# Kernel tuning notes

Hardware: AMD Instinct MI355X
Metric: run time of the kernel (lower is better)

Reference implementation:

```python
import jax, jax.numpy as jnp
import numpy as np

EMBED_DIM = 1024
NUM_HEADS = 16
HEAD_DIM = EMBED_DIM // NUM_HEADS
ROPE_BASE = 10000.0


def rotate_half(x):
    # interleaved variant: pairs (x0,x1) -> (-x1, x0)
    x1 = x[..., ::2]
    x2 = x[..., 1::2]
    return jnp.stack((-x2, x1), axis=-1).reshape(x.shape)


def rope_tables(T, dim, dtype):
    inv_freq = 1.0 / (ROPE_BASE ** (jnp.arange(0, dim, 2, dtype=jnp.float32) / dim))
    t = jnp.arange(T, dtype=jnp.float32)
    freqs = t[:, None] * inv_freq[None, :]          # [T, dim/2]
    emb = jnp.concatenate((freqs, freqs), axis=-1)  # [T, dim]
    return jnp.cos(emb).astype(dtype), jnp.sin(emb).astype(dtype)


def setup_inputs() -> dict:
    key = jax.random.key(0)
    kx, kq, ko = jax.random.split(key, 3)
    B, T, D = 2, 2048, EMBED_DIM
    x = jax.random.normal(kx, (B, T, D), dtype=jnp.float32)
    s = 1.0 / np.sqrt(D)
    Wqkv = jax.random.normal(kq, (D, 3 * D), dtype=jnp.float32) * s
    Wout = jax.random.normal(ko, (D, D), dtype=jnp.float32) * s
    return {"x": x, "Wqkv": Wqkv, "Wout": Wout}


def reference(x, Wqkv, Wout):
    B, T, D = x.shape
    H, hd = NUM_HEADS, HEAD_DIM
    qkv = x @ Wqkv                                   # [B,T,3D]
    q, k, v = jnp.split(qkv, 3, axis=-1)
    q = q.reshape(B, T, H, hd).transpose(0, 2, 1, 3)  # [B,H,T,hd]
    k = k.reshape(B, T, H, hd).transpose(0, 2, 1, 3)
    v = v.reshape(B, T, H, hd).transpose(0, 2, 1, 3)
    cos, sin = rope_tables(T, hd, x.dtype)           # [T,hd]
    cos = cos[None, None, :, :]
    sin = sin[None, None, :, :]
    q = q * cos + rotate_half(q) * sin
    k = k * cos + rotate_half(k) * sin
    scale = 1.0 / np.sqrt(hd).astype(np.float32)
    attn = jnp.einsum('bhtd,bhsd->bhts', q, k) * scale  # [B,H,T,T]
    attn = jax.nn.softmax(attn, axis=-1)
    out = jnp.einsum('bhts,bhsd->bhtd', attn, v)     # [B,H,T,hd]
    out = out.transpose(0, 2, 1, 3).reshape(B, T, D)
    return out @ Wout
```

## Files before the change

kernel.cpp:

```cpp
#include <hip/hip_runtime.h>
#include <hip/hip_bf16.h>
#include <stdint.h>


typedef unsigned short u16;
typedef short bf16x8 __attribute__((ext_vector_type(8)));
typedef float f32x4  __attribute__((ext_vector_type(4)));

#if defined(__has_builtin) && __has_builtin(__builtin_amdgcn_exp2f)
#define EXP2F(x) __builtin_amdgcn_exp2f(x)
#else
#define EXP2F(x) exp2f(x)
#endif

__device__ __forceinline__ u16 f2b(float f) {
  uint32_t u = __float_as_uint(f);
  u += 0x7fffu + ((u >> 16) & 1u);
  return (u16)(u >> 16);
}
__device__ __forceinline__ uint32_t pk2(float a, float b) {
  return (uint32_t)f2b(a) | ((uint32_t)f2b(b) << 16);
}

__device__ __forceinline__ void gl2lds16(const void* g, void* l) {
  __builtin_amdgcn_global_load_lds(
      (const __attribute__((address_space(1))) unsigned int*)g,
      (__attribute__((address_space(3))) unsigned int*)l, 16, 0, 0);
}

__global__ void sniff_kernel(const u16* x, int* flag) {
  __shared__ int cnt;
  if (threadIdx.x == 0) cnt = 0;
  __syncthreads();
  int c = 0;
  for (int i = threadIdx.x; i < 4096; i += 256) {
    float a = fabsf(__uint_as_float(((uint32_t)x[2*i]) << 16));
    if (a > 1e-3f && a < 100.f) c++;
  }
  atomicAdd(&cnt, c);
  __syncthreads();
  if (threadIdx.x == 0) *flag = (cnt > 2048) ? 1 : 0;
}

__global__ __launch_bounds__(256) void convert_x_kernel(
    const void* __restrict__ xv, const int* __restrict__ flag, u16* __restrict__ Xb)
{
  const int isb = *flag;
  const size_t i = ((size_t)blockIdx.x * 256 + threadIdx.x) * 8;
  if (isb) {
    *(uint4*)&Xb[i] = *(const uint4*)((const u16*)xv + i);
  } else {
    const float* s = (const float*)xv + i;
    float4 a = *(const float4*)s, b = *(const float4*)(s + 4);
    uint4 p;
    p.x = pk2(a.x, a.y); p.y = pk2(a.z, a.w);
    p.z = pk2(b.x, b.y); p.w = pk2(b.z, b.w);
    *(uint4*)&Xb[i] = p;
  }
}

__global__ __launch_bounds__(256) void transpose_w_kernel(
    const void* __restrict__ src, u16* __restrict__ dst,
    int K, int N, const int* __restrict__ flag)
{
  __shared__ u16 Lt[64 * 72];
  const int isb = *flag;
  const int tid = threadIdx.x;
  const int n0 = blockIdx.x * 64, k0 = blockIdx.y * 64;
  const int r = tid >> 2, cseg = (tid & 3) << 4;
  u16 t[16];
  if (isb) {
    const u16* s = (const u16*)src + (size_t)(k0 + r) * N + n0 + cseg;
    *(uint4*)&t[0] = *(const uint4*)s;
    *(uint4*)&t[8] = *(const uint4*)(s + 8);
  } else {
    const float* s = (const float*)src + (size_t)(k0 + r) * N + n0 + cseg;
    #pragma unroll
    for (int j = 0; j < 4; j++) {
      float4 v = *(const float4*)(s + j * 4);
      t[j*4+0] = f2b(v.x); t[j*4+1] = f2b(v.y); t[j*4+2] = f2b(v.z); t[j*4+3] = f2b(v.w);
    }
  }
  #pragma unroll
  for (int j = 0; j < 16; j++) Lt[(cseg + j) * 72 + r] = t[j];
  __syncthreads();
  const int n = tid >> 2, kseg = (tid & 3) << 4;
  uint4 u0 = *(const uint4*)&Lt[n * 72 + kseg];
  uint4 u1 = *(const uint4*)&Lt[n * 72 + kseg + 8];
  u16* d = dst + (size_t)(n0 + n) * K + k0 + kseg;
  *(uint4*)d = u0;
  *(uint4*)(d + 8) = u1;
}

__global__ __launch_bounds__(256) void rope_table_kernel(float2* __restrict__ CS) {
  const int idx = blockIdx.x * 256 + threadIdx.x;
  const int t = idx >> 5, f = idx & 31;
  float invf = __expf(-(float)f * 0.2878231366242557f);
  float th = (float)t * invf;
  float sn, cs;
  sincosf(th, &sn, &cs);
  CS[idx] = make_float2(cs, sn);
}

__global__ __launch_bounds__(256) void qkv_kernel(
    const u16* __restrict__ Xb, const u16* __restrict__ Wt,
    const float2* __restrict__ CS,
    u16* __restrict__ Q, u16* __restrict__ K, u16* __restrict__ Vt)
{
  __shared__ u16 As[128 * 64];
  __shared__ u16 Bs[128 * 64];
  const int tid = threadIdx.x;
  const int n0 = blockIdx.x * 128;
  const int m0 = blockIdx.y * 128;
  const int w = tid >> 6, l = tid & 63, lr = l & 15, lq = l >> 4;
  const int mrow0 = (w & 1) * 64;
  const int ncol0 = (w >> 1) * 64;

  const int srow = tid >> 3;
  const int gseg = (tid & 7) ^ (srow & 7);

  f32x4 acc[4][4] = {};

  for (int k0 = 0; k0 < 1024; k0 += 64) {
    __syncthreads();
    #pragma unroll
    for (int rd = 0; rd < 4; rd++) {
      const int row = srow + rd * 32;
      gl2lds16(Xb + (size_t)(m0 + row) * 1024 + k0 + gseg * 8, &As[tid * 8 + rd * 2048]);
      gl2lds16(Wt + (size_t)(n0 + row) * 1024 + k0 + gseg * 8, &Bs[tid * 8 + rd * 2048]);
    }
    __syncthreads();
    #pragma unroll
    for (int kc = 0; kc < 2; kc++) {
      bf16x8 af[4], bf[4];
      #pragma unroll
      for (int i = 0; i < 4; i++) {
        const int seg = ((kc << 2) | lq) ^ (lr & 7);
        af[i] = *(const bf16x8*)&As[(mrow0 + i * 16 + lr) * 64 + seg * 8];
        bf[i] = *(const bf16x8*)&Bs[(ncol0 + i * 16 + lr) * 64 + seg * 8];
      }
      #pragma unroll
      for (int mb = 0; mb < 4; mb++)
        #pragma unroll
        for (int nb = 0; nb < 4; nb++)
          acc[mb][nb] = __builtin_amdgcn_mfma_f32_16x16x32_bf16(af[mb], bf[nb], acc[mb][nb], 0, 0, 0);
    }
  }

  const int col0 = n0 + ncol0;
  const int sec = col0 >> 10;
  const int h = (col0 >> 6) & 15;
  if (sec == 2) {
    #pragma unroll
    for (int mb = 0; mb < 4; mb++) {
      const int row0 = m0 + mrow0 + mb * 16 + lq * 4;
      const int b = row0 >> 11, t0 = row0 & 2047;
      #pragma unroll
      for (int nb = 0; nb < 4; nb++) {
        const int d = nb * 16 + lr;
        uint2 uv;
        uv.x = pk2(acc[mb][nb][0], acc[mb][nb][1]);
        uv.y = pk2(acc[mb][nb][2], acc[mb][nb][3]);
        *(uint2*)&Vt[(((size_t)b * 16 + h) * 64 + d) * 2048 + t0] = uv;
      }
    }
  } else {
    u16* dst = (sec == 0) ? Q : K;
    const float qscale = 0.125f * 1.44269504f;
    #pragma unroll
    for (int mb = 0; mb < 4; mb++) {
      const int row0 = m0 + mrow0 + mb * 16 + lq * 4;
      const int b = row0 >> 11, t0 = row0 & 2047;
      #pragma unroll
      for (int nb = 0; nb < 4; nb++) {
        const int d = nb * 16 + lr;
        const int f = d & 31;
        #pragma unroll
        for (int r = 0; r < 4; r++) {
          const int t = t0 + r;
          float2 cs = CS[t * 32 + f];
          float val = acc[mb][nb][r];
          float prt = __shfl_xor(val, 1, 64);
          float res = fmaf(val, cs.x, ((d & 1) ? prt : -prt) * cs.y);
          if (sec == 0) res *= qscale;
          dst[(((size_t)b * 16 + h) * 2048 + t) * 64 + d] = f2b(res);
        }
      }
    }
  }
}

__global__ __launch_bounds__(256) void attn_kernel(
    const u16* __restrict__ Q, const u16* __restrict__ K,
    const u16* __restrict__ Vt, u16* __restrict__ ATT)
{
  __shared__ u16 Ks[64 * 64];
  __shared__ u16 Vs[64 * 64];
  __shared__ u16 Ps[4 * 32 * 72];
  const int tid = threadIdx.x;
  const int w = tid >> 6, l = tid & 63, lr = l & 15, lq = l >> 4;
  const int bh = blockIdx.x >> 4;
  const int qt = blockIdx.x & 15;
  const size_t base = (size_t)bh * (2048 * 64);
  const int qrow0 = qt * 128 + w * 32;
  u16* Psw = Ps + w * (32 * 72);

  bf16x8 qf[2][2];
  #pragma unroll
  for (int mb = 0; mb < 2; mb++)
    #pragma unroll
    for (int kc = 0; kc < 2; kc++)
      qf[mb][kc] = *(const bf16x8*)(Q + base + (size_t)(qrow0 + mb * 16 + lr) * 64 + kc * 32 + lq * 8);

  f32x4 oa[2][4] = {};
  f32x4 lsum[2] = {};

  const int srow = tid >> 3;
  const int gseg = (tid & 7) ^ (srow & 7);

  #pragma unroll 1
  for (int s0 = 0; s0 < 2048; s0 += 64) {
    __syncthreads();
    #pragma unroll
    for (int rd = 0; rd < 2; rd++) {
      const int row = srow + rd * 32;
      const int gs = (tid & 7) ^ (row & 7);
      gl2lds16(K + base + (size_t)(s0 + row) * 64 + gs * 8, &Ks[tid * 8 + rd * 2048]);
      gl2lds16(Vt + base + (size_t)row * 2048 + s0 + gs * 8, &Vs[tid * 8 + rd * 2048]);
    }
    __syncthreads();

    bf16x8 kf[4][2], vf[4][2];
    #pragma unroll
    for (int nb = 0; nb < 4; nb++)
      #pragma unroll
      for (int kc = 0; kc < 2; kc++) {
        const int seg = ((kc << 2) | lq) ^ (lr & 7);
        kf[nb][kc] = *(const bf16x8*)&Ks[(nb * 16 + lr) * 64 + seg * 8];
        vf[nb][kc] = *(const bf16x8*)&Vs[(nb * 16 + lr) * 64 + seg * 8];
      }

    const int ev = (lr & 1) == 0;
    #pragma unroll
    for (int mb = 0; mb < 2; mb++) {
      #pragma unroll
      for (int nb = 0; nb < 4; nb++) {
        f32x4 s = {};
        s = __builtin_amdgcn_mfma_f32_16x16x32_bf16(qf[mb][0], kf[nb][0], s, 0, 0, 0);
        s = __builtin_amdgcn_mfma_f32_16x16x32_bf16(qf[mb][1], kf[nb][1], s, 0, 0, 0);
        float e0 = EXP2F(s[0]), e1 = EXP2F(s[1]), e2 = EXP2F(s[2]), e3 = EXP2F(s[3]);
        lsum[mb][0] += e0; lsum[mb][1] += e1;
        lsum[mb][2] += e2; lsum[mb][3] += e3;
        uint32_t p01 = (uint32_t)f2b(e0) | ((uint32_t)f2b(e1) << 16);
        uint32_t p23 = (uint32_t)f2b(e2) | ((uint32_t)f2b(e3) << 16);
        uint32_t pp01 = (uint32_t)__shfl_xor((int)p01, 1, 64);
        uint32_t pp23 = (uint32_t)__shfl_xor((int)p23, 1, 64);
        uint32_t wA = ev ? ((p01 & 0xffffu) | (pp01 << 16))
                         : ((pp23 & 0xffffu) | (p23 << 16));
        uint32_t wB = ev ? ((p01 >> 16) | (pp01 & 0xffff0000u))
                         : ((pp23 >> 16) | (p23 & 0xffff0000u));
        const int row0 = mb * 16 + lq * 4 + (ev ? 0 : 2);
        const int c = nb * 16 + (lr & ~1);
        *(uint32_t*)&Psw[row0 * 72 + c] = wA;
        *(uint32_t*)&Psw[(row0 + 1) * 72 + c] = wB;
      }
    }

    #pragma unroll
    for (int mb = 0; mb < 2; mb++) {
      bf16x8 pf0 = *(const bf16x8*)&Psw[(mb * 16 + lr) * 72 + lq * 8];
      bf16x8 pf1 = *(const bf16x8*)&Psw[(mb * 16 + lr) * 72 + 32 + lq * 8];
      #pragma unroll
      for (int nb = 0; nb < 4; nb++) {
        oa[mb][nb] = __builtin_amdgcn_mfma_f32_16x16x32_bf16(pf0, vf[nb][0], oa[mb][nb], 0, 0, 0);
        oa[mb][nb] = __builtin_amdgcn_mfma_f32_16x16x32_bf16(pf1, vf[nb][1], oa[mb][nb], 0, 0, 0);
      }
    }
  }

  const int b = bh >> 4, h = bh & 15;
  #pragma unroll
  for (int mb = 0; mb < 2; mb++) {
    #pragma unroll
    for (int r = 0; r < 4; r++) {
      float v = lsum[mb][r];
      v += __shfl_xor(v, 1, 64);
      v += __shfl_xor(v, 2, 64);
      v += __shfl_xor(v, 4, 64);
      v += __shfl_xor(v, 8, 64);
      lsum[mb][r] = 1.f / v;
    }
    #pragma unroll
    for (int nb = 0; nb < 4; nb++) {
      const int d = nb * 16 + lr;
      #pragma unroll
      for (int r = 0; r < 4; r++) {
        const int t = qrow0 + mb * 16 + lq * 4 + r;
        ATT[((size_t)(b * 2048 + t)) * 1024 + h * 64 + d] = f2b(oa[mb][nb][r] * lsum[mb][r]);
      }
    }
  }
}

__global__ __launch_bounds__(256) void outproj_kernel(
    const u16* __restrict__ A, const u16* __restrict__ Wt,
    const int* __restrict__ flag, void* __restrict__ outv)
{
  __shared__ u16 As[128 * 64];
  __shared__ u16 Bs[128 * 64];
  const int isb = *flag;
  const int tid = threadIdx.x;
  const int n0 = blockIdx.x * 128;
  const int m0 = blockIdx.y * 128;
  const int w = tid >> 6, l = tid & 63, lr = l & 15, lq = l >> 4;
  const int mrow0 = (w & 1) * 64;
  const int ncol0 = (w >> 1) * 64;
  const int srow = tid >> 3;
  const int gseg = (tid & 7) ^ (srow & 7);

  f32x4 acc[4][4] = {};

  for (int k0 = 0; k0 < 1024; k0 += 64) {
    __syncthreads();
    #pragma unroll
    for (int rd = 0; rd < 4; rd++) {
      const int row = srow + rd * 32;
      gl2lds16(A + (size_t)(m0 + row) * 1024 + k0 + gseg * 8, &As[tid * 8 + rd * 2048]);
      gl2lds16(Wt + (size_t)(n0 + row) * 1024 + k0 + gseg * 8, &Bs[tid * 8 + rd * 2048]);
    }
    __syncthreads();
    #pragma unroll
    for (int kc = 0; kc < 2; kc++) {
      bf16x8 af[4], bf[4];
      #pragma unroll
      for (int i = 0; i < 4; i++) {
        const int seg = ((kc << 2) | lq) ^ (lr & 7);
        af[i] = *(const bf16x8*)&As[(mrow0 + i * 16 + lr) * 64 + seg * 8];
        bf[i] = *(const bf16x8*)&Bs[(ncol0 + i * 16 + lr) * 64 + seg * 8];
      }
      #pragma unroll
      for (int mb = 0; mb < 4; mb++)
        #pragma unroll
        for (int nb = 0; nb < 4; nb++)
          acc[mb][nb] = __builtin_amdgcn_mfma_f32_16x16x32_bf16(af[mb], bf[nb], acc[mb][nb], 0, 0, 0);
    }
  }
  #pragma unroll
  for (int mb = 0; mb < 4; mb++) {
    const int row = m0 + mrow0 + mb * 16 + lq * 4;
    #pragma unroll
    for (int nb = 0; nb < 4; nb++) {
      const int col = n0 + ncol0 + nb * 16 + lr;
      #pragma unroll
      for (int r = 0; r < 4; r++) {
        float val = acc[mb][nb][r];
        if (isb) ((u16*)outv)[(size_t)(row + r) * 1024 + col] = f2b(val);
        else     ((float*)outv)[(size_t)(row + r) * 1024 + col] = val;
      }
    }
  }
}

extern "C" void kernel_launch(void* const* d_in, const int* in_sizes, int n_in,
                              void* d_out, int out_size, void* d_ws, size_t ws_size,
                              hipStream_t stream)
{
  const void* x    = d_in[0];
  const void* wqkv = d_in[1];
  const void* wout = d_in[2];
  char* ws = (char*)d_ws;
  const size_t MB = 1024 * 1024;
  int*    flag   = (int*)ws;
  float2* CS     = (float2*)(ws + 1024);
  u16*    Xb     = (u16*)(ws + 1 * MB);
  u16*    ATT    = Xb;
  u16*    Wqkvt  = (u16*)(ws + 9 * MB);
  u16*    Woutt  = (u16*)(ws + 15 * MB);
  u16*    Q      = (u16*)(ws + 17 * MB);
  u16*    K      = (u16*)(ws + 25 * MB);
  u16*    Vt     = (u16*)(ws + 33 * MB);

  sniff_kernel<<<1, 256, 0, stream>>>((const u16*)x, flag);
  convert_x_kernel<<<2048, 256, 0, stream>>>(x, flag, Xb);
  transpose_w_kernel<<<dim3(48, 16), 256, 0, stream>>>(wqkv, Wqkvt, 1024, 3072, flag);
  transpose_w_kernel<<<dim3(16, 16), 256, 0, stream>>>(wout, Woutt, 1024, 1024, flag);
  rope_table_kernel<<<256, 256, 0, stream>>>(CS);
  qkv_kernel<<<dim3(24, 32), 256, 0, stream>>>(Xb, Wqkvt, CS, Q, K, Vt);
  attn_kernel<<<512, 256, 0, stream>>>(Q, K, Vt, ATT);
  outproj_kernel<<<dim3(8, 32), 256, 0, stream>>>(ATT, Woutt, flag, d_out);
}
```

Before: 239.5 us.

## Split attention along keys with double-buffered K/V tiles and a combine pass

Double-buffers the K/V LDS tiles so the next tile's global-to-LDS loads overlap the current tile's compute. It also transposes the MFMA operand order so P is written to LDS without lane shuffles, and converts to bf16 with packed intrinsics. When the workspace is large enough, keys are split in two halves across a second grid dimension, and a combine kernel sums the fp32 partials and normalises them. This doubles block count for occupancy, at the cost of extra fp32 partial traffic and one more launch.

```diff
diff --git a/kernel.cpp b/kernel.cpp
--- a/kernel.cpp
+++ b/kernel.cpp
@@ -20,6 +20,11 @@
 }
 __device__ __forceinline__ uint32_t pk2(float a, float b) {
   return (uint32_t)f2b(a) | ((uint32_t)f2b(b) << 16);
+}
+__device__ __forceinline__ uint32_t pkbf(float a, float b) {
+  __hip_bfloat162 h = __float22bfloat162_rn(make_float2(a, b));
+  union { __hip_bfloat162 h2; uint32_t u; } cv; cv.h2 = h;
+  return cv.u;
 }
 
 __device__ __forceinline__ void gl2lds16(const void* g, void* l) {
@@ -115,7 +120,6 @@
   const int w = tid >> 6, l = tid & 63, lr = l & 15, lq = l >> 4;
   const int mrow0 = (w & 1) * 64;
   const int ncol0 = (w >> 1) * 64;
-
   const int srow = tid >> 3;
   const int gseg = (tid & 7) ^ (srow & 7);
 
@@ -190,20 +194,24 @@
   }
 }
 
-__global__ __launch_bounds__(256) void attn_kernel(
+__global__ __launch_bounds__(256, 3) void attn_kernel(
     const u16* __restrict__ Q, const u16* __restrict__ K,
-    const u16* __restrict__ Vt, u16* __restrict__ ATT)
-{
-  __shared__ u16 Ks[64 * 64];
-  __shared__ u16 Vs[64 * 64];
-  __shared__ u16 Ps[4 * 32 * 72];
+    const u16* __restrict__ Vt, u16* __restrict__ ATT,
+    float* __restrict__ Op, float* __restrict__ Ls)
+{
+  __shared__ u16 Ks[2][64 * 64];
+  __shared__ u16 Vs[2][64 * 64];
+  __shared__ u16 Ps[4][32 * 72];
   const int tid = threadIdx.x;
   const int w = tid >> 6, l = tid & 63, lr = l & 15, lq = l >> 4;
   const int bh = blockIdx.x >> 4;
   const int qt = blockIdx.x & 15;
+  const int ns = gridDim.y, sh = blockIdx.y;
+  const int slen = 2048 / ns;
+  const int sbeg = sh * slen;
   const size_t base = (size_t)bh * (2048 * 64);
   const int qrow0 = qt * 128 + w * 32;
-  u16* Psw = Ps + w * (32 * 72);
+  u16* Psw = &Ps[w][0];
 
   bf16x8 qf[2][2];
   #pragma unroll
@@ -212,23 +220,29 @@
     for (int kc = 0; kc < 2; kc++)
       qf[mb][kc] = *(const bf16x8*)(Q + base + (size_t)(qrow0 + mb * 16 + lr) * 64 + kc * 32 + lq * 8);
 
-  f32x4 oa[2][4] = {};
-  f32x4 lsum[2] = {};
+  f32x4 oa[4][2] = {};
+  float lsum[2] = {0.f, 0.f};
 
   const int srow = tid >> 3;
-  const int gseg = (tid & 7) ^ (srow & 7);
-
-  #pragma unroll 1
-  for (int s0 = 0; s0 < 2048; s0 += 64) {
-    __syncthreads();
+
+  auto stage = [&](int buf, int s0) {
     #pragma unroll
     for (int rd = 0; rd < 2; rd++) {
       const int row = srow + rd * 32;
       const int gs = (tid & 7) ^ (row & 7);
-      gl2lds16(K + base + (size_t)(s0 + row) * 64 + gs * 8, &Ks[tid * 8 + rd * 2048]);
-      gl2lds16(Vt + base + (size_t)row * 2048 + s0 + gs * 8, &Vs[tid * 8 + rd * 2048]);
-    }
+      gl2lds16(K + base + (size_t)(s0 + row) * 64 + gs * 8, &Ks[buf][tid * 8 + rd * 2048]);
+      gl2lds16(Vt + base + (size_t)row * 2048 + s0 + gs * 8, &Vs[buf][tid * 8 + rd * 2048]);
+    }
+  };
+
+  stage(0, sbeg);
+  const int nt = slen >> 6;
+
+  #pragma unroll 1
+  for (int t = 0; t < nt; t++) {
+    const int buf = t & 1;
     __syncthreads();
+    if (t + 1 < nt) stage(buf ^ 1, sbeg + (t + 1) * 64);
 
     bf16x8 kf[4][2], vf[4][2];
     #pragma unroll
@@ -236,33 +250,23 @@
       #pragma unroll
       for (int kc = 0; kc < 2; kc++) {
         const int seg = ((kc << 2) | lq) ^ (lr & 7);
-        kf[nb][kc] = *(const bf16x8*)&Ks[(nb * 16 + lr) * 64 + seg * 8];
-        vf[nb][kc] = *(const bf16x8*)&Vs[(nb * 16 + lr) * 64 + seg * 8];
-      }
-
-    const int ev = (lr & 1) == 0;
-    #pragma unroll
-    for (int mb = 0; mb < 2; mb++) {
-      #pragma unroll
-      for (int nb = 0; nb < 4; nb++) {
-        f32x4 s = {};
-        s = __builtin_amdgcn_mfma_f32_16x16x32_bf16(qf[mb][0], kf[nb][0], s, 0, 0, 0);
-        s = __builtin_amdgcn_mfma_f32_16x16x32_bf16(qf[mb][1], kf[nb][1], s, 0, 0, 0);
-        float e0 = EXP2F(s[0]), e1 = EXP2F(s[1]), e2 = EXP2F(s[2]), e3 = EXP2F(s[3]);
-        lsum[mb][0] += e0; lsum[mb][1] += e1;
-        lsum[mb][2] += e2; lsum[mb][3] += e3;
-        uint32_t p01 = (uint32_t)f2b(e0) | ((uint32_t)f2b(e1) << 16);
-        uint32_t p23 = (uint32_t)f2b(e2) | ((uint32_t)f2b(e3) << 16);
-        uint32_t pp01 = (uint32_t)__shfl_xor((int)p01, 1, 64);
-        uint32_t pp23 = (uint32_t)__shfl_xor((int)p23, 1, 64);
-        uint32_t wA = ev ? ((p01 & 0xffffu) | (pp01 << 16))
-                         : ((pp23 & 0xffffu) | (p23 << 16));
-        uint32_t wB = ev ? ((p01 >> 16) | (pp01 & 0xffff0000u))
-                         : ((pp23 >> 16) | (p23 & 0xffff0000u));
-        const int row0 = mb * 16 + lq * 4 + (ev ? 0 : 2);
-        const int c = nb * 16 + (lr & ~1);
-        *(uint32_t*)&Psw[row0 * 72 + c] = wA;
-        *(uint32_t*)&Psw[(row0 + 1) * 72 + c] = wB;
+        kf[nb][kc] = *(const bf16x8*)&Ks[buf][(nb * 16 + lr) * 64 + seg * 8];
+        vf[nb][kc] = *(const bf16x8*)&Vs[buf][(nb * 16 + lr) * 64 + seg * 8];
+      }
+
+    #pragma unroll
+    for (int sb = 0; sb < 4; sb++) {
+      #pragma unroll
+      for (int mb = 0; mb < 2; mb++) {
+        f32x4 st = {};
+        st = __builtin_amdgcn_mfma_f32_16x16x32_bf16(kf[sb][0], qf[mb][0], st, 0, 0, 0);
+        st = __builtin_amdgcn_mfma_f32_16x16x32_bf16(kf[sb][1], qf[mb][1], st, 0, 0, 0);
+        float e0 = EXP2F(st[0]), e1 = EXP2F(st[1]), e2 = EXP2F(st[2]), e3 = EXP2F(st[3]);
+        lsum[mb] += (e0 + e1) + (e2 + e3);
+        uint2 pp;
+        pp.x = pkbf(e0, e1);
+        pp.y = pkbf(e2, e3);
+        *(uint2*)&Psw[(mb * 16 + lr) * 72 + sb * 16 + lq * 4] = pp;
       }
     }
 
@@ -271,35 +275,69 @@
       bf16x8 pf0 = *(const bf16x8*)&Psw[(mb * 16 + lr) * 72 + lq * 8];
       bf16x8 pf1 = *(const bf16x8*)&Psw[(mb * 16 + lr) * 72 + 32 + lq * 8];
       #pragma unroll
-      for (int nb = 0; nb < 4; nb++) {
-        oa[mb][nb] = __builtin_amdgcn_mfma_f32_16x16x32_bf16(pf0, vf[nb][0], oa[mb][nb], 0, 0, 0);
-        oa[mb][nb] = __builtin_amdgcn_mfma_f32_16x16x32_bf16(pf1, vf[nb][1], oa[mb][nb], 0, 0, 0);
-      }
-    }
-  }
-
-  const int b = bh >> 4, h = bh & 15;
+      for (int db = 0; db < 4; db++) {
+        oa[db][mb] = __builtin_amdgcn_mfma_f32_16x16x32_bf16(vf[db][0], pf0, oa[db][mb], 0, 0, 0);
+        oa[db][mb] = __builtin_amdgcn_mfma_f32_16x16x32_bf16(vf[db][1], pf1, oa[db][mb], 0, 0, 0);
+      }
+    }
+  }
+
   #pragma unroll
   for (int mb = 0; mb < 2; mb++) {
-    #pragma unroll
-    for (int r = 0; r < 4; r++) {
-      float v = lsum[mb][r];
-      v += __shfl_xor(v, 1, 64);
-      v += __shfl_xor(v, 2, 64);
-      v += __shfl_xor(v, 4, 64);
-      v += __shfl_xor(v, 8, 64);
-      lsum[mb][r] = 1.f / v;
-    }
-    #pragma unroll
-    for (int nb = 0; nb < 4; nb++) {
-      const int d = nb * 16 + lr;
-      #pragma unroll
-      for (int r = 0; r < 4; r++) {
-        const int t = qrow0 + mb * 16 + lq * 4 + r;
-        ATT[((size_t)(b * 2048 + t)) * 1024 + h * 64 + d] = f2b(oa[mb][nb][r] * lsum[mb][r]);
-      }
-    }
-  }
+    float v = lsum[mb];
+    v += __shfl_xor(v, 16, 64);
+    v += __shfl_xor(v, 32, 64);
+    lsum[mb] = v;
+  }
+
+  const int b = bh >> 4, h = bh & 15;
+  if (ns == 1) {
+    #pragma unroll
+    for (int mb = 0; mb < 2; mb++) {
+      const float inv = 1.f / lsum[mb];
+      const int t = qrow0 + mb * 16 + lr;
+      u16* dst = ATT + ((size_t)(b * 2048 + t)) * 1024 + h * 64;
+      #pragma unroll
+      for (int db = 0; db < 4; db++) {
+        uint2 u;
+        u.x = pkbf(oa[db][mb][0] * inv, oa[db][mb][1] * inv);
+        u.y = pkbf(oa[db][mb][2] * inv, oa[db][mb][3] * inv);
+        *(uint2*)&dst[db * 16 + lq * 4] = u;
+      }
+    }
+  } else {
+    float* op = Op + (size_t)sh * (65536ull * 64);
+    #pragma unroll
+    for (int mb = 0; mb < 2; mb++) {
+      const size_t row = (size_t)bh * 2048 + qrow0 + mb * 16 + lr;
+      #pragma unroll
+      for (int db = 0; db < 4; db++)
+        *(f32x4*)&op[row * 64 + db * 16 + lq * 4] = oa[db][mb];
+      if (lq == 0) Ls[(size_t)sh * 65536 + row] = lsum[mb];
+    }
+  }
+}
+
+__global__ __launch_bounds__(256) void combine_kernel(
+    const float* __restrict__ Op, const float* __restrict__ Ls, u16* __restrict__ ATT)
+{
+  const int idx = blockIdx.x * 256 + threadIdx.x;
+  const int R = idx >> 3;
+  const int c = (idx & 7) * 8;
+  const float* p0 = Op + (size_t)R * 64 + c;
+  const float* p1 = p0 + 65536ull * 64;
+  f32x4 a0 = *(const f32x4*)p0, a1 = *(const f32x4*)(p0 + 4);
+  f32x4 b0 = *(const f32x4*)p1, b1 = *(const f32x4*)(p1 + 4);
+  const float inv = 1.f / (Ls[R] + Ls[65536 + R]);
+  const int bh = R >> 11, trow = R & 2047;
+  const int b = bh >> 4, h = bh & 15;
+  u16* d = ATT + ((size_t)(b * 2048 + trow)) * 1024 + h * 64 + c;
+  uint4 u;
+  u.x = pkbf((a0[0] + b0[0]) * inv, (a0[1] + b0[1]) * inv);
+  u.y = pkbf((a0[2] + b0[2]) * inv, (a0[3] + b0[3]) * inv);
+  u.z = pkbf((a1[0] + b1[0]) * inv, (a1[1] + b1[1]) * inv);
+  u.w = pkbf((a1[2] + b1[2]) * inv, (a1[3] + b1[3]) * inv);
+  *(uint4*)d = u;
 }
 
 __global__ __launch_bounds__(256) void outproj_kernel(
@@ -379,6 +417,11 @@
   u16*    Q      = (u16*)(ws + 17 * MB);
   u16*    K      = (u16*)(ws + 25 * MB);
   u16*    Vt     = (u16*)(ws + 33 * MB);
+  float*  Op     = (float*)(ws + 41 * MB);
+  float*  Ls     = (float*)(ws + 75 * MB);
+
+  const bool split = ws_size >= 76 * MB;
+  const int ns = split ? 2 : 1;
 
   sniff_kernel<<<1, 256, 0, stream>>>((const u16*)x, flag);
   convert_x_kernel<<<2048, 256, 0, stream>>>(x, flag, Xb);
@@ -386,6 +429,8 @@
   transpose_w_kernel<<<dim3(16, 16), 256, 0, stream>>>(wout, Woutt, 1024, 1024, flag);
   rope_table_kernel<<<256, 256, 0, stream>>>(CS);
   qkv_kernel<<<dim3(24, 32), 256, 0, stream>>>(Xb, Wqkvt, CS, Q, K, Vt);
-  attn_kernel<<<512, 256, 0, stream>>>(Q, K, Vt, ATT);
+  attn_kernel<<<dim3(512, ns), 256, 0, stream>>>(Q, K, Vt, ATT, Op, Ls);
+  if (split)
+    combine_kernel<<<2048, 256, 0, stream>>>(Op, Ls, ATT);
   outproj_kernel<<<dim3(8, 32), 256, 0, stream>>>(ATT, Woutt, flag, d_out);
 }
```

Result: faster. 226.8 us (-5.3%).
